# Kernel optimization log

Measured on AMD Instinct MI355X. Metric: run time of the kernel, lower is better.

## Reference

```python
import jax, jax.numpy as jnp
import numpy as np

A = 32          # num input capsule types
PSIZE = 16      # caps_size (pose matrix 4x4)
MD = 4          # mat_dim = sqrt(caps_size)
NCLS = 10       # output capsules / classes
KF = 5          # routing kernel (final_shape)
KK = KF * KF
KKA = KK * A
ITERS = 3
FINAL_LAMBDA = 0.01
EPS = 1e-12
LN2PI = float(np.log(2.0 * np.pi))
BN_EPS = 1e-5


def unfold(x, k, stride, pad):
    # torch.nn.functional.unfold: [b,C,h,w] -> [b, C*k*k, L], (c, kh, kw) channel-major
    b, c, h, w = x.shape
    if pad:
        x = jnp.pad(x, ((0, 0), (0, 0), (pad, pad), (pad, pad)))
    oh = (h + 2 * pad - k) // stride + 1
    ow = (w + 2 * pad - k) // stride + 1
    cols = jnp.stack([
        jnp.stack([x[:, :, i:i + stride * oh:stride, j:j + stride * ow:stride]
                   for j in range(k)], axis=3)
        for i in range(k)], axis=2)          # [b, c, k, k, oh, ow]
    return cols.reshape(b, c * k * k, oh * ow)


def conv3x3(x, w):
    return jax.lax.conv_general_dilated(x, w, (1, 1), [(1, 1), (1, 1)],
                                        dimension_numbers=('NCHW', 'OIHW', 'NCHW'))


def bn_inf(x, g, b, m, v):
    scale = g / jnp.sqrt(v + BN_EPS)
    return (x - m[None, :, None, None]) * scale[None, :, None, None] + b[None, :, None, None]


def em_routing(a_in, pose, W, beta_u, beta_a):
    b = a_in.shape[0]
    # pose votes
    pu = unfold(pose, KF, 1, 0)                     # [b, A*PSIZE*KK, l]
    l = pu.shape[-1]
    pu = pu.reshape(b, A, PSIZE, KK, l).transpose(0, 4, 3, 1, 2).reshape(b, l, KKA, PSIZE)
    pm = pu.reshape(b, l, KKA, MD, MD)[:, :, :, None]        # [b,l,kkA,1,md,md]
    v = jnp.matmul(pm, W)                                    # [b,l,kkA,B,md,md]
    v = v.reshape(b, l, KKA, NCLS, PSIZE)
    # activations
    au = unfold(a_in, KF, 1, 0).reshape(b, A, KK, l).transpose(0, 3, 2, 1).reshape(b, l, KKA)
    r = jnp.ones((b, l, KKA, NCLS, 1), v.dtype)
    a_out = mu = None
    for i in range(ITERS):
        lam = FINAL_LAMBDA * (1.0 - 0.95 ** (i + 1))
        # M-step
        rw = r * au[:, :, :, None, None]
        r_sum = rw.sum(axis=2, keepdims=True)                # [b,l,1,B,1]
        coeff = rw / (r_sum + EPS)
        mu = (coeff * v).sum(axis=2, keepdims=True)          # [b,l,1,B,psize]
        sigma_sq = (coeff * (v - mu) ** 2).sum(axis=2, keepdims=True) + EPS
        r_s = r_sum[:, :, 0]                                 # [b,l,B,1]
        sig = sigma_sq[:, :, 0]                              # [b,l,B,psize]
        cost_h = (beta_u + 0.5 * jnp.log(sig)) * r_s         # log(sqrt(s)) = 0.5*log(s)
        a_out = jax.nn.sigmoid(lam * (beta_a - cost_h.sum(axis=3)))   # [b,l,B]
        if i < ITERS - 1:
            # E-step (note: log(sigma_sq * ln2pi) as in original code)
            ln_p = (-0.5 * jnp.sum(jnp.log(sigma_sq * LN2PI), axis=-1)
                    - jnp.sum((v - mu) ** 2 / (2.0 * sigma_sq), axis=-1))   # [b,l,kkA,B]
            ln_ap = ln_p + jnp.log(a_out)[:, :, None, :]
            r = jax.nn.softmax(ln_ap, axis=-1)[..., None]
    oh = int(np.floor(np.sqrt(l)))
    pose_out = mu[:, :, 0].reshape(b, l, -1).transpose(0, 2, 1).reshape(b, -1, oh, oh)
    a_map = a_out.transpose(0, 2, 1).reshape(b, -1, oh, oh)
    return a_map, pose_out


def setup_inputs():
    key = jax.random.key(0)
    ks = jax.random.split(key, 14)
    batch = 256
    x = jax.random.normal(ks[0], (batch, 512, 5, 5), jnp.float32)
    w_a = jax.random.normal(ks[1], (A, 512, 3, 3), jnp.float32) * 0.02
    w_pose = jax.random.normal(ks[2], (A * PSIZE, 512, 3, 3), jnp.float32) * 0.02
    bn_a_g = 1.0 + 0.1 * jax.random.normal(ks[3], (A,), jnp.float32)
    bn_a_b = 0.1 * jax.random.normal(ks[4], (A,), jnp.float32)
    bn_a_m = 0.1 * jax.random.normal(ks[5], (A,), jnp.float32)
    bn_a_v = jax.random.uniform(ks[6], (A,), jnp.float32, 0.5, 1.5)
    C2 = A * PSIZE
    bn_p_g = 1.0 + 0.1 * jax.random.normal(ks[7], (C2,), jnp.float32)
    bn_p_b = 0.1 * jax.random.normal(ks[8], (C2,), jnp.float32)
    bn_p_m = 0.1 * jax.random.normal(ks[9], (C2,), jnp.float32)
    bn_p_v = jax.random.uniform(ks[10], (C2,), jnp.float32, 0.5, 1.5)
    W = jax.random.normal(ks[11], (KKA, NCLS, MD, MD), jnp.float32) * 0.25
    beta_u = jnp.zeros((1, 1, NCLS, 1), jnp.float32)
    beta_a = jnp.zeros((1, 1, NCLS), jnp.float32)
    return {"x": x, "w_a": w_a, "w_pose": w_pose,
            "bn_a_g": bn_a_g, "bn_a_b": bn_a_b, "bn_a_m": bn_a_m, "bn_a_v": bn_a_v,
            "bn_p_g": bn_p_g, "bn_p_b": bn_p_b, "bn_p_m": bn_p_m, "bn_p_v": bn_p_v,
            "W": W, "beta_u": beta_u, "beta_a": beta_a}


def reference(x, w_a, w_pose, bn_a_g, bn_a_b, bn_a_m, bn_a_v,
              bn_p_g, bn_p_b, bn_p_m, bn_p_v, W, beta_u, beta_a):
    a = jax.nn.sigmoid(bn_inf(conv3x3(x, w_a), bn_a_g, bn_a_b, bn_a_m, bn_a_v))
    pose = bn_inf(conv3x3(x, w_pose), bn_p_g, bn_p_b, bn_p_m, bn_p_v)
    a_map, _ = em_routing(a, pose, W, beta_u, beta_a)
    out = a_map.reshape(a_map.shape[0], -1)          # [b, 10]
    out = out / out.sum(axis=1, keepdims=True)
    return jnp.log(out)
```

## Files before the change

kernel.cpp:

```cpp
#include <hip/hip_runtime.h>
#include <math.h>

#define CIN 512
#define NCLS 10
#define KDIM 4608
#define NTOT 6400
#define MPAD 640
#define BK 128
#define NKT 36
#define NABLK (5 * NKT)
#define LN2PI_F 1.8378770664093453f

typedef __attribute__((ext_vector_type(8))) short bf16x8;
typedef __attribute__((ext_vector_type(4))) float f32x4;

typedef const __attribute__((address_space(1))) void* gas_ptr;
typedef __attribute__((address_space(3))) void* las_ptr;

__device__ __forceinline__ void async_copy16(const void* g, void* l) {
    __builtin_amdgcn_global_load_lds((gas_ptr)g, (las_ptr)l, 16, 0, 0);
}

__device__ __forceinline__ unsigned short f2bf(float f) {
    unsigned int u = __float_as_uint(f);
    u = (u + 0x7fffu + ((u >> 16) & 1u)) >> 16;
    return (unsigned short)u;
}
__device__ __forceinline__ float bf2f(unsigned short s) {
    return __uint_as_float(((unsigned int)s) << 16);
}
__device__ __forceinline__ float fexp(float x) { return __expf(x); }
__device__ __forceinline__ float flog(float x) { return __logf(x); }

__global__ __launch_bounds__(256) void pack_a_kernel(
    const float* __restrict__ w_pose, const float* __restrict__ w_a,
    const float* __restrict__ bn_p_g, const float* __restrict__ bn_p_b,
    const float* __restrict__ bn_p_m, const float* __restrict__ bn_p_v,
    const float* __restrict__ bn_a_g, const float* __restrict__ bn_a_b,
    const float* __restrict__ bn_a_m, const float* __restrict__ bn_a_v,
    const float* __restrict__ Wm,
    unsigned short* __restrict__ At, unsigned short* __restrict__ Wmb,
    float* __restrict__ sc, float* __restrict__ bi)
{
    const int blk = blockIdx.x;
    const int t = threadIdx.x;

    if (blk >= NABLK) {
        const int chunk = (blk - NABLK) * 256 + t;
        if (chunk < 16000) {
            const float4* s4 = reinterpret_cast<const float4*>(Wm + (size_t)chunk * 8);
            float4 x0 = s4[0], x1 = s4[1];
            int4 o;
            o.x = (int)f2bf(x0.x) | ((int)f2bf(x0.y) << 16);
            o.y = (int)f2bf(x0.z) | ((int)f2bf(x0.w) << 16);
            o.z = (int)f2bf(x1.x) | ((int)f2bf(x1.y) << 16);
            o.w = (int)f2bf(x1.z) | ((int)f2bf(x1.w) << 16);
            reinterpret_cast<int4*>(Wmb + (size_t)chunk * 8)[0] = o;
        }
        return;
    }

    const int mblk = blk / NKT;
    if (blk == 0) {
        for (int i = t; i < MPAD; i += 256) {
            float s = 0.f, b = 0.f;
            if (i < 512) {
                s = bn_p_g[i] / sqrtf(bn_p_v[i] + 1e-5f);
                b = bn_p_b[i] - bn_p_m[i] * s;
            } else if (i < 544) {
                const int j = i - 512;
                s = bn_a_g[j] / sqrtf(bn_a_v[j] + 1e-5f);
                b = bn_a_b[j] - bn_a_m[j] * s;
            }
            sc[i] = s; bi[i] = b;
        }
    }

    const int kt = blk - mblk * NKT;
    #pragma unroll
    for (int j = 0; j < 8; ++j) {
        const int c = t + j * 256;
        const int kc8 = c >> 7, slot = c & 127;
        const int row = mblk * 128 + (slot ^ (kc8 << 2));
        const int k0 = (kt * 16 + kc8) * 8;
        float v[8] = {0.f,0.f,0.f,0.f,0.f,0.f,0.f,0.f};
        if (row < 512) {
            const float4* s4 = reinterpret_cast<const float4*>(w_pose + (size_t)row * KDIM + k0);
            float4 x0 = s4[0], x1 = s4[1];
            v[0]=x0.x; v[1]=x0.y; v[2]=x0.z; v[3]=x0.w;
            v[4]=x1.x; v[5]=x1.y; v[6]=x1.z; v[7]=x1.w;
        } else if (row < 544) {
            const float4* s4 = reinterpret_cast<const float4*>(w_a + (size_t)(row - 512) * KDIM + k0);
            float4 x0 = s4[0], x1 = s4[1];
            v[0]=x0.x; v[1]=x0.y; v[2]=x0.z; v[3]=x0.w;
            v[4]=x1.x; v[5]=x1.y; v[6]=x1.z; v[7]=x1.w;
        }
        int4 o;
        o.x = (int)f2bf(v[0]) | ((int)f2bf(v[1]) << 16);
        o.y = (int)f2bf(v[2]) | ((int)f2bf(v[3]) << 16);
        o.z = (int)f2bf(v[4]) | ((int)f2bf(v[5]) << 16);
        o.w = (int)f2bf(v[6]) | ((int)f2bf(v[7]) << 16);
        reinterpret_cast<int4*>(At + ((((size_t)blk) << 11) + c) * 8)[0] = o;
    }
}

__global__ __launch_bounds__(1024) void pack_b_kernel(
    const float* __restrict__ x, unsigned short* __restrict__ Bt)
{
    __shared__ __align__(16) float xs[CIN * 25];
    const int b = blockIdx.x;
    const int t = threadIdx.x;
    const float4* xb = reinterpret_cast<const float4*>(x + (size_t)b * (CIN * 25));
    for (int f4 = t; f4 < (CIN * 25) / 4; f4 += 1024)
        reinterpret_cast<float4*>(xs)[f4] = xb[f4];
    __syncthreads();

    for (int w = t; w < 25 * (KDIM / 8); w += 1024) {
        const int px = w / (KDIM / 8);
        const int ch = w - px * (KDIM / 8);
        const int py = px / 5, qx = px % 5;
        const int k0 = ch * 8;
        unsigned short v[8];
        #pragma unroll
        for (int j = 0; j < 8; ++j) {
            const int k = k0 + j;
            const int ci = k / 9;
            const int kk = k - ci * 9;
            const int dy = kk / 3, dx = kk - dy * 3;
            const int yy = py + dy - 1, xx = qx + dx - 1;
            const bool ok = (yy >= 0) & (yy < 5) & (xx >= 0) & (xx < 5);
            v[j] = ok ? f2bf(xs[ci * 25 + yy * 5 + xx]) : (unsigned short)0;
        }
        int4 o;
        o.x = (int)v[0] | ((int)v[1] << 16);
        o.y = (int)v[2] | ((int)v[3] << 16);
        o.z = (int)v[4] | ((int)v[5] << 16);
        o.w = (int)v[6] | ((int)v[7] << 16);
        const int n = b * 25 + px;
        const int nblk = n >> 7, nr = n & 127;
        const int kt = k0 >> 7;
        const int kc8 = (k0 >> 3) & 15;
        const int c = kc8 * 128 + (nr ^ (kc8 << 2));
        reinterpret_cast<int4*>(Bt + ((((size_t)(nblk * NKT + kt)) << 11) + c) * 8)[0] = o;
    }
}

__global__ __launch_bounds__(512) void gemm_kernel(
    const unsigned short* __restrict__ At,
    const unsigned short* __restrict__ Bt,
    const float* __restrict__ sc, const float* __restrict__ bi,
    unsigned short* __restrict__ Cp,
    float* __restrict__ Ca)
{
    __shared__ __align__(16) unsigned char smem[131072];
    const int t = threadIdx.x;
    const int L = blockIdx.x;
    int mblk, nblk;
    if (L >= 240) { const int i = L - 240; mblk = i >> 1; nblk = 48 + (i & 1); }
    else          { const int q = L / 40, r = L - q * 40;
                    mblk = r >> 3; nblk = q * 8 + (r & 7); }
    const int m0 = mblk * 128, n0 = nblk * 128;
    const int lane = t & 63, w = t >> 6;
    const int g = w >> 2, wq = w & 3;
    const int wm = wq >> 1, wn = wq & 1;
    const int row16 = lane & 15, quad = lane >> 4;

    f32x4 acc[4][4] = {};

    const unsigned short* gAbase = At + (((size_t)mblk * NKT) << 14);
    const unsigned short* gBbase = Bt + (((size_t)nblk * NKT) << 14);

    #define STAGE(kt, s)                                                      \
    {                                                                         \
        unsigned short* As_ = (unsigned short*)(smem + (s) * 65536);          \
        unsigned short* Bs_ = As_ + 16384;                                    \
        const unsigned short* ga = gAbase + ((size_t)(kt) << 14);             \
        const unsigned short* gb = gBbase + ((size_t)(kt) << 14);             \
        _Pragma("unroll")                                                     \
        for (int j = 0; j < 4; ++j) {                                         \
            async_copy16(ga + ((size_t)(j * 512 + t) << 3),                   \
                         As_ + ((size_t)(j * 512 + w * 64) << 3));            \
            async_copy16(gb + ((size_t)(j * 512 + t) << 3),                   \
                         Bs_ + ((size_t)(j * 512 + w * 64) << 3));            \
        }                                                                     \
    }

    #define COMPUTE(s)                                                        \
    {                                                                         \
        const unsigned short* As_ = (const unsigned short*)(smem + (s) * 65536);\
        const unsigned short* Bs_ = As_ + 16384;                              \
        _Pragma("unroll")                                                     \
        for (int ks = 0; ks < 2; ++ks) {                                      \
            const int kc8b = g * 8 + ks * 4 + quad;                           \
            const int sw = kc8b << 2;                                         \
            bf16x8 af[4], bfr[4];                                             \
            _Pragma("unroll")                                                 \
            for (int mt = 0; mt < 4; ++mt)                                    \
                af[mt] = *reinterpret_cast<const bf16x8*>(                    \
                    &As_[(size_t)(kc8b * 128 + ((wm * 64 + mt * 16 + row16) ^ sw)) * 8]);\
            _Pragma("unroll")                                                 \
            for (int nt = 0; nt < 4; ++nt)                                    \
                bfr[nt] = *reinterpret_cast<const bf16x8*>(                   \
                    &Bs_[(size_t)(kc8b * 128 + ((wn * 64 + nt * 16 + row16) ^ sw)) * 8]);\
            _Pragma("unroll")                                                 \
            for (int mt = 0; mt < 4; ++mt)                                    \
                _Pragma("unroll")                                             \
                for (int nt = 0; nt < 4; ++nt)                                \
                    acc[mt][nt] = __builtin_amdgcn_mfma_f32_16x16x32_bf16(    \
                        af[mt], bfr[nt], acc[mt][nt], 0, 0, 0);               \
        }                                                                     \
    }

    STAGE(0, 0);
    for (int kt = 0; kt < NKT; ++kt) {
        __syncthreads();
        if (kt + 1 < NKT) STAGE(kt + 1, (kt + 1) & 1);
        COMPUTE(kt & 1);
    }
    #undef STAGE
    #undef COMPUTE

    float* mb = (float*)smem;
    #pragma unroll
    for (int rnd = 0; rnd < 2; ++rnd) {
        __syncthreads();
        if (g == 1 && (wq >> 1) == rnd) {
            f32x4* dst = (f32x4*)(mb + (wq & 1) * 4096);
            #pragma unroll
            for (int i = 0; i < 16; ++i)
                dst[i * 64 + lane] = acc[i >> 2][i & 3];
        }
        __syncthreads();
        if (g == 0 && (wq >> 1) == rnd) {
            const f32x4* src = (const f32x4*)(mb + (wq & 1) * 4096);
            #pragma unroll
            for (int i = 0; i < 16; ++i)
                acc[i >> 2][i & 3] += src[i * 64 + lane];
        }
    }

    if (g == 0) {
        #pragma unroll
        for (int mt = 0; mt < 4; ++mt) {
            const int mbase = m0 + wm * 64 + mt * 16 + quad * 4;
            if (mbase >= 544) continue;
            #pragma unroll
            for (int rg = 0; rg < 4; ++rg) {
                const int m = mbase + rg;
                const float s = sc[m], bbx = bi[m];
                #pragma unroll
                for (int nt = 0; nt < 4; ++nt) {
                    const int n = n0 + wn * 64 + nt * 16 + row16;
                    const float v = fmaf(acc[mt][nt][rg], s, bbx);
                    if (m < 512) Cp[(size_t)m * NTOT + n] = f2bf(v);
                    else Ca[(size_t)(m - 512) * NTOT + n] = 1.f / (1.f + fexp(-v));
                }
            }
        }
    }
}

__device__ __forceinline__ void loadW_bf(const unsigned short* wp, float* wv) {
    const int4* q = reinterpret_cast<const int4*>(wp);
    const int4 q0 = q[0], q1 = q[1];
    const unsigned int u[8] = {(unsigned)q0.x,(unsigned)q0.y,(unsigned)q0.z,(unsigned)q0.w,
                               (unsigned)q1.x,(unsigned)q1.y,(unsigned)q1.z,(unsigned)q1.w};
    #pragma unroll
    for (int i = 0; i < 8; ++i) {
        wv[2*i]   = __uint_as_float(u[i] << 16);
        wv[2*i+1] = __uint_as_float(u[i] & 0xFFFF0000u);
    }
}

__global__ __launch_bounds__(640, 1) void em_kernel(
    const unsigned short* __restrict__ Cp,
    const float* __restrict__ Ca,
    const unsigned short* __restrict__ Wmb,
    const float* __restrict__ beta_u, const float* __restrict__ beta_a,
    float* __restrict__ out)
{
    __shared__ __align__(16) float psh[25][32][20];
    __shared__ float aush[800];
    __shared__ float lnqp[2][NCLS][800];
    __shared__ float mu_sh[NCLS][16];
    __shared__ float i2s_sh[NCLS][16];
    __shared__ float costp[2][NCLS];
    __shared__ float slgp[2][NCLS];
    __shared__ float Kc_sh[NCLS];
    __shared__ float aout_sh[NCLS];

    const int b = blockIdx.x, t = threadIdx.x;
    const int rh = (t >= 320) ? 1 : 0;
    const int th = t - rh * 320;
    const int c = th >> 5, a = th & 31;
    float* rwsh = &lnqp[1][0][0];

    const unsigned short* pb = Cp + (size_t)b * 25;
    for (int f = t; f < 12800; f += 640) {
        const int c2 = f / 25, px = f - c2 * 25;
        psh[px][c2 >> 4][c2 & 15] = bf2f(pb[(size_t)c2 * NTOT + px]);
    }
    const float* ab = Ca + (size_t)b * 25;
    for (int f = t; f < 800; f += 640) {
        const int ci = f / 25, px = f - ci * 25;
        aush[px * 32 + ci] = ab[(size_t)ci * NTOT + px];
    }
    __syncthreads();

    const float bu = beta_u[c], ba = beta_a[c];
    float muL[8], i2sL[8], KcL = 0.f;
    const unsigned short* wbase = Wmb + ((size_t)a * NCLS + c) * 16;

    #define VOTE_HALF(kk, vv)                                                \
        float pm[8], wv[16];                                                 \
        {                                                                    \
            const float4* pr = reinterpret_cast<const float4*>(&psh[kk][a][rh * 8]); \
            const float4 p0 = pr[0], p1 = pr[1];                             \
            pm[0]=p0.x; pm[1]=p0.y; pm[2]=p0.z; pm[3]=p0.w;                  \
            pm[4]=p1.x; pm[5]=p1.y; pm[6]=p1.z; pm[7]=p1.w;                  \
            loadW_bf(wbase + (size_t)(kk) * 5120, wv);                       \
            _Pragma("unroll")                                                \
            for (int jr = 0; jr < 2; ++jr) {                                 \
                _Pragma("unroll")                                            \
                for (int s = 0; s < 4; ++s) {                                \
                    float av = 0.f;                                          \
                    _Pragma("unroll")                                        \
                    for (int tt = 0; tt < 4; ++tt)                           \
                        av = fmaf(pm[jr*4+tt], wv[tt*4+s], av);              \
                    vv[jr*4+s] = av;                                         \
                }                                                            \
            }                                                                \
        }

    float p95 = 1.f;
    for (int it = 0; it < 3; ++it) {
        p95 *= 0.95f;
        const float lam = 0.01f * (1.f - p95);

        if (it > 0) {
            for (int kk = 0; kk < 25; ++kk) {
                float vv[8];
                VOTE_HALF(kk, vv);
                float q = (rh == 0) ? KcL : 0.f;
                #pragma unroll
                for (int j = 0; j < 8; ++j) {
                    const float d = vv[j] - muL[j];
                    q -= d * d * i2sL[j];
                }
                lnqp[rh][c][kk * 32 + a] = q;
            }
            __syncthreads();
            {
                float* l0 = &lnqp[0][0][0];
                const float* l1 = &lnqp[1][0][0];
                for (int f = t; f < 8000; f += 640) l0[f] += l1[f];
            }
            __syncthreads();
            {
                const int k0 = rh ? 13 : 0, k1 = rh ? 25 : 13;
                for (int kk = k0; kk < k1; ++kk) {
                    const int m = kk * 32 + a;
                    float qv[NCLS];
                    #pragma unroll
                    for (int cc = 0; cc < NCLS; ++cc) qv[cc] = lnqp[0][cc][m];
                    float mx = qv[0];
                    #pragma unroll
                    for (int cc = 1; cc < NCLS; ++cc) mx = fmaxf(mx, qv[cc]);
                    float den = 0.f;
                    #pragma unroll
                    for (int cc = 0; cc < NCLS; ++cc) den += fexp(qv[cc] - mx);
                    rwsh[c * 800 + m] = fexp(qv[c] - mx) * __builtin_amdgcn_rcpf(den)
                                        * aush[m];
                }
            }
            __syncthreads();
        }

        float S0 = 0.f, S1[8], S2[8];
        #pragma unroll
        for (int j = 0; j < 8; ++j) { S1[j] = 0.f; S2[j] = 0.f; }

        for (int kk = 0; kk < 25; ++kk) {
            float vv[8];
            VOTE_HALF(kk, vv);
            const int m = kk * 32 + a;
            const float rw = (it == 0) ? aush[m] : rwsh[c * 800 + m];
            S0 += rw;
            #pragma unroll
            for (int j = 0; j < 8; ++j) {
                const float rv = rw * vv[j];
                S1[j] += rv;
                S2[j] = fmaf(rv, vv[j], S2[j]);
            }
        }

        #pragma unroll
        for (int off = 16; off >= 1; off >>= 1) {
            S0 += __shfl_xor(S0, off);
            #pragma unroll
            for (int j = 0; j < 8; ++j) {
                S1[j] += __shfl_xor(S1[j], off);
                S2[j] += __shfl_xor(S2[j], off);
            }
        }

        if (a == 0) {
            const float s0e = S0 + 1e-12f;
            const float inv = 1.f / s0e;
            float cost_ = 0.f, slg_ = 0.f;
            #pragma unroll
            for (int j = 0; j < 8; ++j) {
                const float mu_ = S1[j] * inv;
                const float sg = (S2[j] - 2.f * mu_ * S1[j] + mu_ * mu_ * S0) * inv
                                 + 1e-12f;
                cost_ += bu + 0.5f * flog(sg);
                slg_ += flog(sg * LN2PI_F);
                mu_sh[c][rh * 8 + j] = mu_;
                i2s_sh[c][rh * 8 + j] = 0.5f / sg;
            }
            costp[rh][c] = cost_;
            slgp[rh][c] = slg_;
        }
        __syncthreads();
        if (a == 0 && rh == 0) {
            const float costsum = (costp[0][c] + costp[1][c]) * S0;
            const float aout = 1.f / (1.f + fexp(-(lam * (ba - costsum))));
            aout_sh[c] = aout;
            Kc_sh[c] = flog(aout) - 0.5f * (slgp[0][c] + slgp[1][c]);
        }
        __syncthreads();
        if (it < 2) {
            #pragma unroll
            for (int j = 0; j < 8; ++j) {
                muL[j] = mu_sh[c][rh * 8 + j];
                i2sL[j] = i2s_sh[c][rh * 8 + j];
            }
            KcL = Kc_sh[c];
        }
    }

    if (t < NCLS) {
        float s = 0.f;
        #pragma unroll
        for (int cc = 0; cc < NCLS; ++cc) s += aout_sh[cc];
        out[b * NCLS + t] = flog(aout_sh[t] / s);
    }
    #undef VOTE_HALF
}

extern "C" void kernel_launch(void* const* d_in, const int* in_sizes, int n_in,
                              void* d_out, int out_size, void* d_ws, size_t ws_size,
                              hipStream_t stream) {
    const float* x      = (const float*)d_in[0];
    const float* w_a    = (const float*)d_in[1];
    const float* w_pose = (const float*)d_in[2];
    const float* bn_a_g = (const float*)d_in[3];
    const float* bn_a_b = (const float*)d_in[4];
    const float* bn_a_m = (const float*)d_in[5];
    const float* bn_a_v = (const float*)d_in[6];
    const float* bn_p_g = (const float*)d_in[7];
    const float* bn_p_b = (const float*)d_in[8];
    const float* bn_p_m = (const float*)d_in[9];
    const float* bn_p_v = (const float*)d_in[10];
    const float* Wm     = (const float*)d_in[11];
    const float* beta_u = (const float*)d_in[12];
    const float* beta_a = (const float*)d_in[13];
    float* out = (float*)d_out;

    char* p = (char*)d_ws;
    unsigned short* At  = (unsigned short*)p;  p += (size_t)MPAD * KDIM * 2;
    unsigned short* Bt  = (unsigned short*)p;  p += (size_t)NTOT * KDIM * 2;
    unsigned short* Wmb = (unsigned short*)p;  p += (size_t)800 * NCLS * 16 * 2;
    unsigned short* Cp  = (unsigned short*)p;  p += (size_t)512 * NTOT * 2;
    float* Ca = (float*)p;                     p += (size_t)32 * NTOT * 4;
    float* sc = (float*)p;                     p += MPAD * 4;
    float* bi = (float*)p;                     p += MPAD * 4;

    pack_a_kernel<<<NABLK + 63, 256, 0, stream>>>(w_pose, w_a,
                                                  bn_p_g, bn_p_b, bn_p_m, bn_p_v,
                                                  bn_a_g, bn_a_b, bn_a_m, bn_a_v,
                                                  Wm, At, Wmb, sc, bi);
    pack_b_kernel<<<256, 1024, 0, stream>>>(x, Bt);
    gemm_kernel<<<250, 512, 0, stream>>>(At, Bt, sc, bi, Cp, Ca);
    em_kernel<<<256, 640, 0, stream>>>(Cp, Ca, Wmb, beta_u, beta_a, out);
}
```

Baseline: 258.0 us.

## Pack EM votes with float2 math, prefetch W and pose, reorder pack_b indexing

Rewrites the EM-routing vote and accumulation loops to use two-wide float vectors, which can map to packed FP32 instructions (v_pk_fma/v_pk_mul). The W weights are software-prefetched one to two iterations ahead, and the pose and routing-weight LDS reads one iteration ahead, to hide global and LDS latency. It also swaps the work-index decomposition in pack_b so consecutive threads walk pixels instead of channel chunks, which changes the shared-memory and global-store access pattern. The prefetch buffers raise register pressure in a kernel launched with 640 threads and one block per SM.

```diff
diff --git a/kernel.cpp b/kernel.cpp
--- a/kernel.cpp
+++ b/kernel.cpp
@@ -13,6 +13,7 @@
 
 typedef __attribute__((ext_vector_type(8))) short bf16x8;
 typedef __attribute__((ext_vector_type(4))) float f32x4;
+typedef __attribute__((ext_vector_type(2))) float f32x2;
 
 typedef const __attribute__((address_space(1))) void* gas_ptr;
 typedef __attribute__((address_space(3))) void* las_ptr;
@@ -116,8 +117,8 @@
     __syncthreads();
 
     for (int w = t; w < 25 * (KDIM / 8); w += 1024) {
-        const int px = w / (KDIM / 8);
-        const int ch = w - px * (KDIM / 8);
+        const int ch = w / 25;
+        const int px = w - ch * 25;
         const int py = px / 5, qx = px % 5;
         const int k0 = ch * 8;
         unsigned short v[8];
@@ -260,15 +261,30 @@
     }
 }
 
-__device__ __forceinline__ void loadW_bf(const unsigned short* wp, float* wv) {
-    const int4* q = reinterpret_cast<const int4*>(wp);
-    const int4 q0 = q[0], q1 = q[1];
+__device__ __forceinline__ void unpackW2(const int4& q0, const int4& q1, f32x2* wv2) {
     const unsigned int u[8] = {(unsigned)q0.x,(unsigned)q0.y,(unsigned)q0.z,(unsigned)q0.w,
                                (unsigned)q1.x,(unsigned)q1.y,(unsigned)q1.z,(unsigned)q1.w};
     #pragma unroll
     for (int i = 0; i < 8; ++i) {
-        wv[2*i]   = __uint_as_float(u[i] << 16);
-        wv[2*i+1] = __uint_as_float(u[i] & 0xFFFF0000u);
+        f32x2 p;
+        p.x = __uint_as_float(u[i] << 16);
+        p.y = __uint_as_float(u[i] & 0xFFFF0000u);
+        wv2[i] = p;
+    }
+}
+
+__device__ __forceinline__ void vote_half2(const float* pm, const f32x2* wv2, f32x2* v2) {
+    #pragma unroll
+    for (int jr = 0; jr < 2; ++jr) {
+        f32x2 vA = {0.f, 0.f}, vB = {0.f, 0.f};
+        #pragma unroll
+        for (int tt = 0; tt < 4; ++tt) {
+            const f32x2 pb = {pm[jr*4+tt], pm[jr*4+tt]};
+            vA += pb * wv2[tt*2+0];
+            vB += pb * wv2[tt*2+1];
+        }
+        v2[jr*2+0] = vA;
+        v2[jr*2+1] = vB;
     }
 }
 
@@ -308,29 +324,9 @@
     __syncthreads();
 
     const float bu = beta_u[c], ba = beta_a[c];
-    float muL[8], i2sL[8], KcL = 0.f;
+    f32x2 mu2[4], i2s2[4];
+    float KcL = 0.f;
     const unsigned short* wbase = Wmb + ((size_t)a * NCLS + c) * 16;
-
-    #define VOTE_HALF(kk, vv)                                                \
-        float pm[8], wv[16];                                                 \
-        {                                                                    \
-            const float4* pr = reinterpret_cast<const float4*>(&psh[kk][a][rh * 8]); \
-            const float4 p0 = pr[0], p1 = pr[1];                             \
-            pm[0]=p0.x; pm[1]=p0.y; pm[2]=p0.z; pm[3]=p0.w;                  \
-            pm[4]=p1.x; pm[5]=p1.y; pm[6]=p1.z; pm[7]=p1.w;                  \
-            loadW_bf(wbase + (size_t)(kk) * 5120, wv);                       \
-            _Pragma("unroll")                                                \
-            for (int jr = 0; jr < 2; ++jr) {                                 \
-                _Pragma("unroll")                                            \
-                for (int s = 0; s < 4; ++s) {                                \
-                    float av = 0.f;                                          \
-                    _Pragma("unroll")                                        \
-                    for (int tt = 0; tt < 4; ++tt)                           \
-                        av = fmaf(pm[jr*4+tt], wv[tt*4+s], av);              \
-                    vv[jr*4+s] = av;                                         \
-                }                                                            \
-            }                                                                \
-        }
 
     float p95 = 1.f;
     for (int it = 0; it < 3; ++it) {
@@ -338,16 +334,28 @@
         const float lam = 0.01f * (1.f - p95);
 
         if (it > 0) {
+            int4 wr0 = *reinterpret_cast<const int4*>(wbase);
+            int4 wr1 = *reinterpret_cast<const int4*>(wbase + 8);
             for (int kk = 0; kk < 25; ++kk) {
-                float vv[8];
-                VOTE_HALF(kk, vv);
-                float q = (rh == 0) ? KcL : 0.f;
+                const int4 w0 = wr0, w1 = wr1;
+                if (kk < 24) {
+                    const unsigned short* wn = wbase + (size_t)(kk + 1) * 5120;
+                    wr0 = *reinterpret_cast<const int4*>(wn);
+                    wr1 = *reinterpret_cast<const int4*>(wn + 8);
+                }
+                const float4* pr = reinterpret_cast<const float4*>(&psh[kk][a][rh * 8]);
+                const float4 p0 = pr[0], p1 = pr[1];
+                const float pm[8] = {p0.x,p0.y,p0.z,p0.w, p1.x,p1.y,p1.z,p1.w};
+                f32x2 wv2[8], v2[4];
+                unpackW2(w0, w1, wv2);
+                vote_half2(pm, wv2, v2);
+                f32x2 acc = {0.f, 0.f};
                 #pragma unroll
-                for (int j = 0; j < 8; ++j) {
-                    const float d = vv[j] - muL[j];
-                    q -= d * d * i2sL[j];
+                for (int jp = 0; jp < 4; ++jp) {
+                    const f32x2 d = v2[jp] - mu2[jp];
+                    acc += d * d * i2s2[jp];
                 }
-                lnqp[rh][c][kk * 32 + a] = q;
+                lnqp[rh][c][kk * 32 + a] = ((rh == 0) ? KcL : 0.f) - acc.x - acc.y;
             }
             __syncthreads();
             {
@@ -376,31 +384,56 @@
             __syncthreads();
         }
 
-        float S0 = 0.f, S1[8], S2[8];
-        #pragma unroll
-        for (int j = 0; j < 8; ++j) { S1[j] = 0.f; S2[j] = 0.f; }
-
+        const float* rwp = (it == 0) ? aush : &lnqp[1][0][0] + c * 800;
+        float S0 = 0.f;
+        f32x2 S1[4] = {}, S2[4] = {};
+
+        int4 wA0 = *reinterpret_cast<const int4*>(wbase);
+        int4 wA1 = *reinterpret_cast<const int4*>(wbase + 8);
+        int4 wB0 = *reinterpret_cast<const int4*>(wbase + 5120);
+        int4 wB1 = *reinterpret_cast<const int4*>(wbase + 5120 + 8);
+        float4 pr0 = *reinterpret_cast<const float4*>(&psh[0][a][rh * 8]);
+        float4 pr1 = *reinterpret_cast<const float4*>(&psh[0][a][rh * 8 + 4]);
+        float rwC = rwp[a];
         for (int kk = 0; kk < 25; ++kk) {
-            float vv[8];
-            VOTE_HALF(kk, vv);
-            const int m = kk * 32 + a;
-            const float rw = (it == 0) ? aush[m] : rwsh[c * 800 + m];
+            const int4 w0 = wA0, w1 = wA1;
+            const float4 p0 = pr0, p1 = pr1;
+            const float rw = rwC;
+            const int k2 = (kk + 2 < 24) ? kk + 2 : 24;
+            const int k1 = (kk + 1 < 24) ? kk + 1 : 24;
+            wA0 = wB0; wA1 = wB1;
+            {
+                const unsigned short* wn = wbase + (size_t)k2 * 5120;
+                wB0 = *reinterpret_cast<const int4*>(wn);
+                wB1 = *reinterpret_cast<const int4*>(wn + 8);
+            }
+            pr0 = *reinterpret_cast<const float4*>(&psh[k1][a][rh * 8]);
+            pr1 = *reinterpret_cast<const float4*>(&psh[k1][a][rh * 8 + 4]);
+            rwC = rwp[k1 * 32 + a];
+
+            const float pm[8] = {p0.x,p0.y,p0.z,p0.w, p1.x,p1.y,p1.z,p1.w};
+            f32x2 wv2[8], v2[4];
+            unpackW2(w0, w1, wv2);
+            vote_half2(pm, wv2, v2);
             S0 += rw;
-            #pragma unroll
-            for (int j = 0; j < 8; ++j) {
-                const float rv = rw * vv[j];
-                S1[j] += rv;
-                S2[j] = fmaf(rv, vv[j], S2[j]);
-            }
-        }
-
+            const f32x2 rw2 = {rw, rw};
+            #pragma unroll
+            for (int jp = 0; jp < 4; ++jp) {
+                const f32x2 rv = rw2 * v2[jp];
+                S1[jp] += rv;
+                S2[jp] += rv * v2[jp];
+            }
+        }
+
+        float* S1f = reinterpret_cast<float*>(S1);
+        float* S2f = reinterpret_cast<float*>(S2);
         #pragma unroll
         for (int off = 16; off >= 1; off >>= 1) {
             S0 += __shfl_xor(S0, off);
             #pragma unroll
             for (int j = 0; j < 8; ++j) {
-                S1[j] += __shfl_xor(S1[j], off);
-                S2[j] += __shfl_xor(S2[j], off);
+                S1f[j] += __shfl_xor(S1f[j], off);
+                S2f[j] += __shfl_xor(S2f[j], off);
             }
         }
 
@@ -410,8 +443,8 @@
             float cost_ = 0.f, slg_ = 0.f;
             #pragma unroll
             for (int j = 0; j < 8; ++j) {
-                const float mu_ = S1[j] * inv;
-                const float sg = (S2[j] - 2.f * mu_ * S1[j] + mu_ * mu_ * S0) * inv
+                const float mu_ = S1f[j] * inv;
+                const float sg = (S2f[j] - 2.f * mu_ * S1f[j] + mu_ * mu_ * S0) * inv
                                  + 1e-12f;
                 cost_ += bu + 0.5f * flog(sg);
                 slg_ += flog(sg * LN2PI_F);
@@ -431,9 +464,13 @@
         __syncthreads();
         if (it < 2) {
             #pragma unroll
-            for (int j = 0; j < 8; ++j) {
-                muL[j] = mu_sh[c][rh * 8 + j];
-                i2sL[j] = i2s_sh[c][rh * 8 + j];
+            for (int jp = 0; jp < 4; ++jp) {
+                f32x2 m2, s2;
+                m2.x = mu_sh[c][rh * 8 + jp * 2];
+                m2.y = mu_sh[c][rh * 8 + jp * 2 + 1];
+                s2.x = i2s_sh[c][rh * 8 + jp * 2];
+                s2.y = i2s_sh[c][rh * 8 + jp * 2 + 1];
+                mu2[jp] = m2; i2s2[jp] = s2;
             }
             KcL = Kc_sh[c];
         }
@@ -445,7 +482,6 @@
         for (int cc = 0; cc < NCLS; ++cc) s += aout_sh[cc];
         out[b * NCLS + t] = flog(aout_sh[t] / s);
     }
-    #undef VOTE_HALF
 }
 
 extern "C" void kernel_launch(void* const* d_in, const int* in_sizes, int n_in,
```

Measured after the change: 240.8 us. 1.07x faster.
